# Kernel tuning notes

Measured on AMD Instinct MI355X. Metric: run time of the kernel, lower is better.

## Reference

```python
import jax, jax.numpy as jnp
import numpy as np

N_ENT, N_REL, E_DIM, R_DIM, K, B = 100000, 64, 128, 128, 32, 16384


def _lookup_maxnorm(table, ids):
    # torch nn.Embedding(max_norm=1): rows with L2 norm > 1 are renormed to 1 at lookup
    x = table[ids]
    n = jnp.linalg.norm(x, axis=-1, keepdims=True)
    return x * jnp.minimum(1.0, 1.0 / jnp.maximum(n, 1e-12))


def setup_inputs() -> dict:
    key = jax.random.key(0)
    ks = jax.random.split(key, 10)
    xavier = lambda k, shp: jax.random.uniform(k, shp, jnp.float32, -1.0, 1.0) * np.sqrt(6.0 / (shp[0] + shp[1]))
    return {
        "idx": jax.random.randint(ks[0], (B,), 0, N_ENT),
        "adj_ent": jax.random.randint(ks[1], (N_ENT, K), 0, N_ENT),
        "adj_rel": jax.random.randint(ks[2], (N_ENT, K), 0, N_REL),
        "ent_table": xavier(ks[3], (N_ENT, E_DIM)),
        "rel_table": xavier(ks[4], (N_REL, R_DIM)),
        "Wr_w": xavier(ks[5], (R_DIM, E_DIM)),
        "Wr_b": jnp.zeros((R_DIM,), jnp.float32),
        "W1_w": xavier(ks[6], (E_DIM, E_DIM)),
        "W1_b": jnp.zeros((E_DIM,), jnp.float32),
        "W2_w": xavier(ks[7], (E_DIM, E_DIM)),
        "W2_b": jnp.zeros((E_DIM,), jnp.float32),
    }


def reference(idx, adj_ent, adj_rel, ent_table, rel_table, Wr_w, Wr_b, W1_w, W1_b, W2_w, W2_b):
    idx = jnp.clip(idx, 0, N_ENT - 1)
    e_ids = adj_ent[idx]                      # [B, K]
    r_ids = adj_rel[idx]                      # [B, K]
    t = _lookup_maxnorm(ent_table, e_ids)     # [B, K, E]
    r = _lookup_maxnorm(rel_table, r_ids)     # [B, K, R]
    h = _lookup_maxnorm(ent_table, idx)       # [B, E]
    # GAT message pass
    hr = h @ Wr_w.T + Wr_b                    # [B, R]
    tr = t @ Wr_w.T + Wr_b                    # [B, K, R]
    score = jnp.sum(jnp.tanh(hr[:, None, :] + r) * tr, axis=-1, keepdims=True)  # [B, K, 1]
    att = jax.nn.softmax(score, axis=1)
    Nh = jnp.sum(t * att, axis=1)             # [B, E]
    # Bi-Interaction aggregate
    leaky = lambda x: jax.nn.leaky_relu(x, 0.2)
    return leaky((h + Nh) @ W1_w.T + W1_b) + leaky((h * Nh) @ W2_w.T + W2_b)
```

## Files before the change

kernel.cpp:

```cpp
#include <hip/hip_runtime.h>
#include <hip/hip_fp16.h>
#include <math.h>

#define N_ENT 100000
#define N_REL 64
#define DIM   128
#define KNB   32
#define BATCH 16384
#define STRIPS (N_ENT / 16)

typedef _Float16 f16;
typedef __attribute__((ext_vector_type(2))) _Float16 f16x2;
typedef __attribute__((ext_vector_type(8))) _Float16 f16x8;
typedef __attribute__((ext_vector_type(4))) float floatx4;

__device__ __forceinline__ int clamp_id(int id) {
    return id < 0 ? 0 : (id > N_ENT - 1 ? N_ENT - 1 : id);
}

__device__ __forceinline__ f16x2 h2v(__half2 h) {
    union { __half2 h; f16x2 v; } u; u.h = h; return u.v;
}

__global__ __launch_bounds__(256) void k_small(
    const float* __restrict__ Wr, const float* __restrict__ W1,
    const float* __restrict__ W2, f16* __restrict__ Wr16,
    f16* __restrict__ W116, f16* __restrict__ W216,
    const float* __restrict__ rel, __half2* __restrict__ REL2)
{
    if (blockIdx.x < 64) {
        const int t = blockIdx.x * 256 + threadIdx.x;
        Wr16[t] = (f16)Wr[t];
        W116[t] = (f16)W1[t];
        W216[t] = (f16)W2[t];
    } else {
        const int lane = threadIdx.x & 63;
        const int row  = (blockIdx.x - 64) * 4 + (threadIdx.x >> 6);
        const float2 x = *(const float2*)(rel + row * DIM + 2 * lane);
        float ss = x.x * x.x + x.y * x.y;
        #pragma unroll
        for (int m = 1; m < 64; m <<= 1) ss += __shfl_xor(ss, m);
        const float s = fminf(1.0f, 1.0f / fmaxf(sqrtf(ss), 1e-12f));
        REL2[row * 64 + lane] = __floats2half2_rn(x.x * s, x.y * s);
    }
}

__global__ __launch_bounds__(256, 4) void k_pre(
    const float* __restrict__ ent, const f16* __restrict__ B,
    const float* __restrict__ bias, f16* __restrict__ TR16,
    f16* __restrict__ N16)
{
    __shared__ f16 Bs[32 * 512];
    const int wid  = threadIdx.x >> 6;
    const int lane = threadIdx.x & 63;
    const int m = lane & 15, quad = lane >> 4;

    #pragma unroll
    for (int i = 0; i < 8; ++i) {
        const int s  = wid * 8 + i;
        const int ct = s >> 2, kt = s & 3;
        const f16* gsrc = B + (size_t)(ct * 16 + m) * DIM + kt * 32 + quad * 8;
        __builtin_amdgcn_global_load_lds(
            (const __attribute__((address_space(1))) unsigned int*)gsrc,
            (__attribute__((address_space(3))) unsigned int*)(Bs + s * 512),
            16, 0, 0);
    }

    const int wstrip = (blockIdx.x * 4 + wid) * 2;
    const int s0 = wstrip     < STRIPS ? wstrip     : STRIPS - 1;
    const int s1 = wstrip + 1 < STRIPS ? wstrip + 1 : STRIPS - 1;

    const float* __restrict__ src0 = ent + (size_t)(s0 * 16 + m) * DIM + quad * 8;
    const float* __restrict__ src1 = ent + (size_t)(s1 * 16 + m) * DIM + quad * 8;
    float x0[4][8], x1[4][8];
    #pragma unroll
    for (int kt = 0; kt < 4; ++kt) {
        *(float4*)&x0[kt][0] = *(const float4*)(src0 + kt * 32);
        *(float4*)&x0[kt][4] = *(const float4*)(src0 + kt * 32 + 4);
    }
    #pragma unroll
    for (int kt = 0; kt < 4; ++kt) {
        *(float4*)&x1[kt][0] = *(const float4*)(src1 + kt * 32);
        *(float4*)&x1[kt][4] = *(const float4*)(src1 + kt * 32 + 4);
    }
    __builtin_amdgcn_sched_barrier(0);

    float ss0 = 0.0f;
    #pragma unroll
    for (int kt = 0; kt < 4; ++kt)
        #pragma unroll
        for (int j = 0; j < 8; ++j) ss0 = fmaf(x0[kt][j], x0[kt][j], ss0);
    ss0 += __shfl_xor(ss0, 16);
    ss0 += __shfl_xor(ss0, 32);
    const float sc0 = fminf(1.0f, 1.0f / fmaxf(sqrtf(ss0), 1e-12f));
    f16x8 a0[4];
    {
        f16* __restrict__ ndst = N16 + (size_t)(s0 * 16 + m) * DIM + quad * 8;
        #pragma unroll
        for (int kt = 0; kt < 4; ++kt) {
            f16x8 av;
            #pragma unroll
            for (int j = 0; j < 8; ++j) av[j] = (f16)(x0[kt][j] * sc0);
            a0[kt] = av;
            *(f16x8*)(ndst + kt * 32) = av;
        }
    }

    float ss1 = 0.0f;
    #pragma unroll
    for (int kt = 0; kt < 4; ++kt)
        #pragma unroll
        for (int j = 0; j < 8; ++j) ss1 = fmaf(x1[kt][j], x1[kt][j], ss1);
    ss1 += __shfl_xor(ss1, 16);
    ss1 += __shfl_xor(ss1, 32);
    const float sc1 = fminf(1.0f, 1.0f / fmaxf(sqrtf(ss1), 1e-12f));
    f16x8 a1[4];
    {
        f16* __restrict__ ndst = N16 + (size_t)(s1 * 16 + m) * DIM + quad * 8;
        #pragma unroll
        for (int kt = 0; kt < 4; ++kt) {
            f16x8 av;
            #pragma unroll
            for (int j = 0; j < 8; ++j) av[j] = (f16)(x1[kt][j] * sc1);
            a1[kt] = av;
            *(f16x8*)(ndst + kt * 32) = av;
        }
    }

    __syncthreads();

    #pragma unroll
    for (int ct = 0; ct < 8; ++ct) {
        floatx4 acc0 = {0.0f, 0.0f, 0.0f, 0.0f};
        floatx4 acc1 = {0.0f, 0.0f, 0.0f, 0.0f};
        #pragma unroll
        for (int kt = 0; kt < 4; ++kt) {
            const f16x8 b = *(const f16x8*)(Bs + (ct * 4 + kt) * 512 + lane * 8);
            acc0 = __builtin_amdgcn_mfma_f32_16x16x32_f16(a0[kt], b, acc0, 0, 0, 0);
            acc1 = __builtin_amdgcn_mfma_f32_16x16x32_f16(a1[kt], b, acc1, 0, 0, 0);
        }
        const float bb = bias[ct * 16 + m];
        #pragma unroll
        for (int r = 0; r < 4; ++r) {
            TR16[(size_t)(s0 * 16 + quad * 4 + r) * DIM + ct * 16 + m] = (f16)(acc0[r] + bb);
            TR16[(size_t)(s1 * 16 + quad * 4 + r) * DIM + ct * 16 + m] = (f16)(acc1[r] + bb);
        }
    }
}

__global__ __launch_bounds__(1024, 8) void k_sag(
    const int* __restrict__ idx, const int* __restrict__ adj_ent,
    const int* __restrict__ adj_rel, const __half2* __restrict__ TR2,
    const __half2* __restrict__ N2, const __half2* __restrict__ REL2,
    const f16* __restrict__ W1h, const float* __restrict__ b1,
    const f16* __restrict__ W2h, const float* __restrict__ b2,
    float* __restrict__ out)
{
    __shared__ f16 Us[16 * DIM];
    __shared__ f16 Vs[16 * DIM];
    const int wid  = threadIdx.x >> 6;
    const int lane = threadIdx.x & 63;
    const int row0 = blockIdx.x * 16;

    const __half2 C1 = __float2half2_rn(-0.33333334f);
    const __half2 C2 = __float2half2_rn(0.13333334f);

    {
        const int r = wid;
        const int b = row0 + r;
        const int id = clamp_id(idx[b]);
        const __half2 hr2 = TR2[(size_t)id * 64 + lane];
        const float2 h  = __half22float2(N2[(size_t)id * 64 + lane]);
        const int eL = adj_ent[(size_t)id * KNB + (lane & 31)];
        const int rL = adj_rel[(size_t)id * KNB + (lane & 31)];

        unsigned int tnd[KNB];
        #pragma unroll
        for (int k = 0; k < KNB; ++k) {
            const int e = __builtin_amdgcn_readlane(eL, k);
            tnd[k] = *((const unsigned int*)N2 + (size_t)e * 64 + lane);
        }

        float p[KNB];
        #pragma unroll
        for (int k = 0; k < KNB; ++k) {
            const int e = __builtin_amdgcn_readlane(eL, k);
            const int rr = __builtin_amdgcn_readlane(rL, k);
            const __half2 tr2 = TR2[(size_t)e * 64 + lane];
            const __half2 rn2 = REL2[rr * 64 + lane];
            const __half2 x  = __hadd2(hr2, rn2);
            const __half2 xx = __hmul2(x, x);
            __half2 q = __hfma2(xx, C2, C1);
            q = __hmul2(q, xx);
            const __half2 mm = __hfma2(x, q, x);
#if __has_builtin(__builtin_amdgcn_fdot2)
            p[k] = __builtin_amdgcn_fdot2(h2v(mm), h2v(tr2), 0.0f, false);
#else
            const float2 mf = __half22float2(mm);
            const float2 tf = __half22float2(tr2);
            p[k] = mf.x * tf.x + mf.y * tf.y;
#endif
        }

        #pragma unroll
        for (int step = 0; step < 5; ++step) {
            const int half = 16 >> step;
            const int mask = 1 << step;
            const bool hi_lane = (lane & mask) != 0;
            #pragma unroll
            for (int i = 0; i < 16; ++i) {
                if (i >= half) break;
                const float lo = p[i], hi = p[i + half];
                const float send = hi_lane ? lo : hi;
                const float recv = __shfl_xor(send, mask);
                p[i] = (hi_lane ? hi : lo) + recv;
            }
        }
        const float sc = p[0] + __shfl_xor(p[0], 32);

        const float ex = __expf(sc);
        float tt = ex;
        #pragma unroll
        for (int m2 = 1; m2 < 32; m2 <<= 1) tt += __shfl_xor(tt, m2);
        const float attL = ex * __builtin_amdgcn_rcpf(tt);

        float nh0 = 0.0f, nh1 = 0.0f;
        #pragma unroll
        for (int k = 0; k < KNB; ++k) {
            const float a = __uint_as_float(
                __builtin_amdgcn_readlane(__float_as_uint(attL), k));
            const float2 t = __half22float2(*(const __half2*)&tnd[k]);
            nh0 = fmaf(a, t.x, nh0);
            nh1 = fmaf(a, t.y, nh1);
        }

        const int chunk = lane >> 2;
        const int boff = r * 256 + ((chunk ^ (r & 7)) << 4) + (lane & 3) * 4;
        *(__half2*)((char*)Us + boff) = __floats2half2_rn(h.x + nh0, h.y + nh1);
        *(__half2*)((char*)Vs + boff) = __floats2half2_rn(h.x * nh0, h.y * nh1);
    }

    __syncthreads();

    if (wid < 8) {
        const int m = lane & 15, quad = lane >> 4;
        f16x8 au[4], av[4];
        #pragma unroll
        for (int kt = 0; kt < 4; ++kt) {
            const int off = m * 256 + (((kt * 4 + quad) ^ (m & 7)) << 4);
            au[kt] = *(const f16x8*)((const char*)Us + off);
            av[kt] = *(const f16x8*)((const char*)Vs + off);
        }

        const int ct = wid;
        floatx4 accU = {0.0f, 0.0f, 0.0f, 0.0f};
        floatx4 accV = {0.0f, 0.0f, 0.0f, 0.0f};
        #pragma unroll
        for (int kt = 0; kt < 4; ++kt) {
            const f16x8 bu = *(const f16x8*)(W1h + (size_t)(ct * 16 + m) * DIM + kt * 32 + quad * 8);
            const f16x8 bv = *(const f16x8*)(W2h + (size_t)(ct * 16 + m) * DIM + kt * 32 + quad * 8);
            accU = __builtin_amdgcn_mfma_f32_16x16x32_f16(au[kt], bu, accU, 0, 0, 0);
            accV = __builtin_amdgcn_mfma_f32_16x16x32_f16(av[kt], bv, accV, 0, 0, 0);
        }
        const float bb1 = b1[ct * 16 + m];
        const float bb2 = b2[ct * 16 + m];
        #pragma unroll
        for (int r = 0; r < 4; ++r) {
            const float x = accU[r] + bb1;
            const float y = accV[r] + bb2;
            const float lx = x > 0.0f ? x : 0.2f * x;
            const float ly = y > 0.0f ? y : 0.2f * y;
            out[(size_t)(row0 + quad * 4 + r) * DIM + ct * 16 + m] = lx + ly;
        }
    }
}

extern "C" void kernel_launch(void* const* d_in, const int* in_sizes, int n_in,
                              void* d_out, int out_size, void* d_ws, size_t ws_size,
                              hipStream_t stream) {
    (void)in_sizes; (void)n_in; (void)out_size; (void)ws_size;
    const int*   idx     = (const int*)d_in[0];
    const int*   adj_ent = (const int*)d_in[1];
    const int*   adj_rel = (const int*)d_in[2];
    const float* ent     = (const float*)d_in[3];
    const float* rel     = (const float*)d_in[4];
    const float* Wr_w    = (const float*)d_in[5];
    const float* Wr_b    = (const float*)d_in[6];
    const float* W1_w    = (const float*)d_in[7];
    const float* W1_b    = (const float*)d_in[8];
    const float* W2_w    = (const float*)d_in[9];
    const float* W2_b    = (const float*)d_in[10];
    float* out = (float*)d_out;

    char* ws = (char*)d_ws;
    f16* N16   = (f16*)(ws);
    f16* TR16  = (f16*)(ws + 25600000);
    f16* REL16 = (f16*)(ws + 51200000);
    f16* Wr16  = (f16*)(ws + 59604992);
    f16* W116  = (f16*)(ws + 59637760);
    f16* W216  = (f16*)(ws + 59670528);

    k_small<<<dim3(80), dim3(256), 0, stream>>>(Wr_w, W1_w, W2_w, Wr16, W116, W216,
                                                rel, (__half2*)REL16);
    k_pre<<<dim3((STRIPS + 7) / 8), dim3(256), 0, stream>>>(ent, Wr16, Wr_b,
                                                            TR16, N16);
    k_sag<<<dim3(BATCH / 16), dim3(1024), 0, stream>>>(idx, adj_ent, adj_rel,
                                                       (const __half2*)TR16,
                                                       (const __half2*)N16,
                                                       (const __half2*)REL16,
                                                       W116, W1_b, W216, W2_b,
                                                       out);
}
```

Baseline: 179.0 us.

## Interleave normalized entity and projected rows into one table for single-load gathers

The separate normalized-entity (N16) and projected (TR16) fp16 tables are merged into one 512-byte-per-row interleaved table, where each lane's 8 bytes hold its N pair and its TR pair. The gather kernel then fetches both values for each neighbor with a single 8-byte load instead of two 4-byte loads from different tables, halving scattered transactions. The neighbor loads and score computation are fused into one loop. The cost is that the precompute kernel now writes narrower strided 4-byte and 2-byte stores instead of 16-byte vector stores.

```diff
diff --git a/kernel.cpp b/kernel.cpp
--- a/kernel.cpp
+++ b/kernel.cpp
@@ -20,6 +20,9 @@
 
 __device__ __forceinline__ f16x2 h2v(__half2 h) {
     union { __half2 h; f16x2 v; } u; u.h = h; return u.v;
+}
+__device__ __forceinline__ __half2 u2h(unsigned int x) {
+    union { unsigned int u; __half2 h; } c; c.u = x; return c.h;
 }
 
 __global__ __launch_bounds__(256) void k_small(
@@ -47,8 +50,7 @@
 
 __global__ __launch_bounds__(256, 4) void k_pre(
     const float* __restrict__ ent, const f16* __restrict__ B,
-    const float* __restrict__ bias, f16* __restrict__ TR16,
-    f16* __restrict__ N16)
+    const float* __restrict__ bias, char* __restrict__ ntb)
 {
     __shared__ f16 Bs[32 * 512];
     const int wid  = threadIdx.x >> 6;
@@ -95,14 +97,19 @@
     const float sc0 = fminf(1.0f, 1.0f / fmaxf(sqrtf(ss0), 1e-12f));
     f16x8 a0[4];
     {
-        f16* __restrict__ ndst = N16 + (size_t)(s0 * 16 + m) * DIM + quad * 8;
+        char* nrow = ntb + (size_t)(s0 * 16 + m) * 512;
         #pragma unroll
         for (int kt = 0; kt < 4; ++kt) {
             f16x8 av;
             #pragma unroll
             for (int j = 0; j < 8; ++j) av[j] = (f16)(x0[kt][j] * sc0);
             a0[kt] = av;
-            *(f16x8*)(ndst + kt * 32) = av;
+            #pragma unroll
+            for (int p = 0; p < 4; ++p) {
+                union { f16x2 v; __half2 h; } c;
+                c.v = (f16x2){av[2 * p], av[2 * p + 1]};
+                *(__half2*)(nrow + (size_t)(kt * 16 + quad * 4 + p) * 8) = c.h;
+            }
         }
     }
 
@@ -116,14 +123,19 @@
     const float sc1 = fminf(1.0f, 1.0f / fmaxf(sqrtf(ss1), 1e-12f));
     f16x8 a1[4];
     {
-        f16* __restrict__ ndst = N16 + (size_t)(s1 * 16 + m) * DIM + quad * 8;
+        char* nrow = ntb + (size_t)(s1 * 16 + m) * 512;
         #pragma unroll
         for (int kt = 0; kt < 4; ++kt) {
             f16x8 av;
             #pragma unroll
             for (int j = 0; j < 8; ++j) av[j] = (f16)(x1[kt][j] * sc1);
             a1[kt] = av;
-            *(f16x8*)(ndst + kt * 32) = av;
+            #pragma unroll
+            for (int p = 0; p < 4; ++p) {
+                union { f16x2 v; __half2 h; } c;
+                c.v = (f16x2){av[2 * p], av[2 * p + 1]};
+                *(__half2*)(nrow + (size_t)(kt * 16 + quad * 4 + p) * 8) = c.h;
+            }
         }
     }
 
@@ -140,18 +152,21 @@
             acc1 = __builtin_amdgcn_mfma_f32_16x16x32_f16(a1[kt], b, acc1, 0, 0, 0);
         }
         const float bb = bias[ct * 16 + m];
+        const size_t coff = (size_t)(ct * 8 + (m >> 1)) * 8 + 4 + (m & 1) * 2;
         #pragma unroll
         for (int r = 0; r < 4; ++r) {
-            TR16[(size_t)(s0 * 16 + quad * 4 + r) * DIM + ct * 16 + m] = (f16)(acc0[r] + bb);
-            TR16[(size_t)(s1 * 16 + quad * 4 + r) * DIM + ct * 16 + m] = (f16)(acc1[r] + bb);
+            char* trow = ntb + (size_t)(s0 * 16 + quad * 4 + r) * 512;
+            *(f16*)(trow + coff) = (f16)(acc0[r] + bb);
+            char* trow1 = ntb + (size_t)(s1 * 16 + quad * 4 + r) * 512;
+            *(f16*)(trow1 + coff) = (f16)(acc1[r] + bb);
         }
     }
 }
 
 __global__ __launch_bounds__(1024, 8) void k_sag(
     const int* __restrict__ idx, const int* __restrict__ adj_ent,
-    const int* __restrict__ adj_rel, const __half2* __restrict__ TR2,
-    const __half2* __restrict__ N2, const __half2* __restrict__ REL2,
+    const int* __restrict__ adj_rel, const char* __restrict__ nt,
+    const __half2* __restrict__ REL2,
     const f16* __restrict__ W1h, const float* __restrict__ b1,
     const f16* __restrict__ W2h, const float* __restrict__ b2,
     float* __restrict__ out)
@@ -169,24 +184,21 @@
         const int r = wid;
         const int b = row0 + r;
         const int id = clamp_id(idx[b]);
-        const __half2 hr2 = TR2[(size_t)id * 64 + lane];
-        const float2 h  = __half22float2(N2[(size_t)id * 64 + lane]);
+        const uint2 pr0 = *(const uint2*)(nt + (size_t)id * 512 + lane * 8);
+        const float2 h  = __half22float2(u2h(pr0.x));
+        const __half2 hr2 = u2h(pr0.y);
         const int eL = adj_ent[(size_t)id * KNB + (lane & 31)];
         const int rL = adj_rel[(size_t)id * KNB + (lane & 31)];
 
-        unsigned int tnd[KNB];
+        unsigned int nds[KNB];
+        float p[KNB];
         #pragma unroll
         for (int k = 0; k < KNB; ++k) {
-            const int e = __builtin_amdgcn_readlane(eL, k);
-            tnd[k] = *((const unsigned int*)N2 + (size_t)e * 64 + lane);
-        }
-
-        float p[KNB];
-        #pragma unroll
-        for (int k = 0; k < KNB; ++k) {
-            const int e = __builtin_amdgcn_readlane(eL, k);
+            const int e  = __builtin_amdgcn_readlane(eL, k);
             const int rr = __builtin_amdgcn_readlane(rL, k);
-            const __half2 tr2 = TR2[(size_t)e * 64 + lane];
+            const uint2 pr = *(const uint2*)(nt + (size_t)e * 512 + lane * 8);
+            nds[k] = pr.x;
+            const __half2 tr2 = u2h(pr.y);
             const __half2 rn2 = REL2[rr * 64 + lane];
             const __half2 x  = __hadd2(hr2, rn2);
             const __half2 xx = __hmul2(x, x);
@@ -229,7 +241,7 @@
         for (int k = 0; k < KNB; ++k) {
             const float a = __uint_as_float(
                 __builtin_amdgcn_readlane(__float_as_uint(attL), k));
-            const float2 t = __half22float2(*(const __half2*)&tnd[k]);
+            const float2 t = __half22float2(u2h(nds[k]));
             nh0 = fmaf(a, t.x, nh0);
             nh1 = fmaf(a, t.y, nh1);
         }
@@ -293,21 +305,17 @@
     float* out = (float*)d_out;
 
     char* ws = (char*)d_ws;
-    f16* N16   = (f16*)(ws);
-    f16* TR16  = (f16*)(ws + 25600000);
-    f16* REL16 = (f16*)(ws + 51200000);
-    f16* Wr16  = (f16*)(ws + 59604992);
-    f16* W116  = (f16*)(ws + 59637760);
-    f16* W216  = (f16*)(ws + 59670528);
+    char* NT    = ws;
+    f16* REL16  = (f16*)(ws + 51200000);
+    f16* Wr16   = (f16*)(ws + 51216384);
+    f16* W116   = (f16*)(ws + 51249152);
+    f16* W216   = (f16*)(ws + 51281920);
 
     k_small<<<dim3(80), dim3(256), 0, stream>>>(Wr_w, W1_w, W2_w, Wr16, W116, W216,
                                                 rel, (__half2*)REL16);
-    k_pre<<<dim3((STRIPS + 7) / 8), dim3(256), 0, stream>>>(ent, Wr16, Wr_b,
-                                                            TR16, N16);
+    k_pre<<<dim3((STRIPS + 7) / 8), dim3(256), 0, stream>>>(ent, Wr16, Wr_b, NT);
     k_sag<<<dim3(BATCH / 16), dim3(1024), 0, stream>>>(idx, adj_ent, adj_rel,
-                                                       (const __half2*)TR16,
-                                                       (const __half2*)N16,
-                                                       (const __half2*)REL16,
+                                                       NT, (const __half2*)REL16,
                                                        W116, W1_b, W216, W2_b,
                                                        out);
 }
```

Result: slower. 246.6 us (+37.8%).
